# Performance work log

Measured on AMD Instinct MI355X. Metric: run time of the kernel, lower is better.

The kernel has to match this reference:

```python
import jax, jax.numpy as jnp
import numpy as np

B, S, D, H = 2, 2048, 1024, 16
DK = D // H  # 64


def setup_inputs() -> dict:
    key = jax.random.key(0)
    ks = jax.random.split(key, 5)
    query_input = jax.random.normal(ks[0], (B, S, D), dtype=jnp.float32)
    # additive mask: 1.0 where attention is disallowed (causal upper triangle)
    mask = jnp.triu(jnp.ones((S, S), dtype=jnp.float32), k=1)[None, None, :, :]
    scale = 1.0 / np.sqrt(D)
    wq = jax.random.normal(ks[1], (D, D), dtype=jnp.float32) * scale
    wk = jax.random.normal(ks[2], (D, D), dtype=jnp.float32) * scale
    wv = jax.random.normal(ks[3], (D, D), dtype=jnp.float32) * scale
    wo = jax.random.normal(ks[4], (D, D), dtype=jnp.float32) * scale
    return {"query_input": query_input, "mask": mask, "wq": wq, "wk": wk, "wv": wv, "wo": wo}


def _split_heads(x):
    # [B, S, D] -> [B, H, S, DK]
    b, s, _ = x.shape
    return x.reshape(b, s, H, DK).transpose(0, 2, 1, 3)


def reference(query_input, mask, wq, wk, wv, wo):
    # self-attention: key_input = value_input = query_input
    q = _split_heads(query_input @ wq)  # [B, H, S, DK]
    k = _split_heads(query_input @ wk)
    v = _split_heads(query_input @ wv)
    scores = jnp.einsum('bhqd,bhkd->bhqk', q, k) / jnp.sqrt(jnp.float32(DK))
    scores = scores + mask * (-1e9)
    attn = jax.nn.softmax(scores, axis=-1)
    out = jnp.einsum('bhqk,bhkd->bhqd', attn, v)  # [B, H, S, DK]
    out = out.transpose(0, 2, 1, 3).reshape(query_input.shape[0], -1, D)
    return out @ wo
```

## Files before the change

kernel.cpp:

```cpp
#include <hip/hip_runtime.h>

typedef __attribute__((ext_vector_type(8))) short bf16x8;
typedef __attribute__((ext_vector_type(4))) float f32x4;
typedef __attribute__((ext_vector_type(4))) unsigned short u16x4;

#define S_LEN 2048
#define D_DIM 1024
#define NHEAD 16
#define DK 64
#define BH 32
#define MROWS 4096

__device__ __forceinline__ unsigned short f2bf(float f) {
    unsigned int u = __float_as_uint(f);
    u += 0x7fffu + ((u >> 16) & 1u);
    return (unsigned short)(u >> 16);
}

__device__ __forceinline__ unsigned int pk_bf16(float a, float b) {
    unsigned int r;
    asm("v_cvt_pk_bf16_f32 %0, %1, %2" : "=v"(r) : "v"(a), "v"(b));
    return r;
}

__device__ __forceinline__ float fexp2(float x) {
    return __builtin_amdgcn_exp2f(x);
}

__device__ __forceinline__ void gload16(const void* g, void* l) {
    __builtin_amdgcn_global_load_lds(
        (const __attribute__((address_space(1))) void*)g,
        (__attribute__((address_space(3))) void*)l, 16, 0, 0);
}

__global__ __launch_bounds__(256) void cast_x_kernel(const float* __restrict__ X,
                                                     unsigned short* __restrict__ Xb) {
    int idx = blockIdx.x * 256 + threadIdx.x;
    float4 v = ((const float4*)X)[idx];
    u16x4 o;
    o.x = f2bf(v.x); o.y = f2bf(v.y); o.z = f2bf(v.z); o.w = f2bf(v.w);
    ((u16x4*)Xb)[idx] = o;
}

__global__ __launch_bounds__(256) void wtrans_kernel(const float* __restrict__ wq,
                                                     const float* __restrict__ wk,
                                                     const float* __restrict__ wv,
                                                     const float* __restrict__ wo,
                                                     unsigned short* __restrict__ Wt) {
    int z = blockIdx.z;
    const float* W = (z == 0) ? wq : (z == 1) ? wk : (z == 2) ? wv : wo;
    unsigned short* O = Wt + (size_t)z * D_DIM * D_DIM;
    __shared__ float t[32][33];
    int tx = threadIdx.x, ty = threadIdx.y;
    int bx = blockIdx.x * 32;
    int by = blockIdx.y * 32;
#pragma unroll
    for (int i = 0; i < 4; ++i)
        t[ty + i * 8][tx] = W[(size_t)(by + ty + i * 8) * D_DIM + bx + tx];
    __syncthreads();
#pragma unroll
    for (int i = 0; i < 4; ++i)
        O[(size_t)(bx + ty + i * 8) * D_DIM + by + tx] = f2bf(t[tx][ty + i * 8]);
}

__device__ __forceinline__ void gemm_mainloop(const unsigned short* __restrict__ A,
                                              const unsigned short* __restrict__ Bt,
                                              int K, int m0, int n0,
                                              unsigned short* As, unsigned short* Bs,
                                              f32x4 acc[4][4]) {
    const int tid = threadIdx.x;
    const int lane = tid & 63, wid = tid >> 6;
    const int wr = wid >> 1, wc = wid & 1;
    const int fr = lane & 15, fk = (lane >> 4) * 8;
    const int nt = K >> 5;
#pragma unroll
    for (int c = 0; c < 2; ++c) {
        int idx = c * 256 + tid;
        int row = idx >> 2;
        int col = (idx & 3) * 8;
        int base = (c * 256 + wid * 64) * 8;
        gload16(&A[(size_t)(m0 + row) * K + col], &As[base]);
        gload16(&Bt[(size_t)(n0 + row) * K + col], &Bs[base]);
    }
    __syncthreads();
    int buf = 0;
    for (int t = 0; t < nt; ++t) {
        if (t + 1 < nt) {
            int k0 = (t + 1) * 32;
#pragma unroll
            for (int c = 0; c < 2; ++c) {
                int idx = c * 256 + tid;
                int row = idx >> 2;
                int col = (idx & 3) * 8;
                int base = ((buf ^ 1) * 512 + c * 256 + wid * 64) * 8;
                gload16(&A[(size_t)(m0 + row) * K + k0 + col], &As[base]);
                gload16(&Bt[(size_t)(n0 + row) * K + k0 + col], &Bs[base]);
            }
        }
        const unsigned short* Ab = As + buf * 512 * 8;
        const unsigned short* Bb = Bs + buf * 512 * 8;
        bf16x8 af[4], bfr[4];
#pragma unroll
        for (int i = 0; i < 4; ++i)
            af[i] = *(const bf16x8*)&Ab[(wr * 64 + i * 16 + fr) * 32 + fk];
#pragma unroll
        for (int j = 0; j < 4; ++j)
            bfr[j] = *(const bf16x8*)&Bb[(wc * 64 + j * 16 + fr) * 32 + fk];
#pragma unroll
        for (int i = 0; i < 4; ++i)
#pragma unroll
            for (int j = 0; j < 4; ++j)
                acc[i][j] = __builtin_amdgcn_mfma_f32_16x16x32_bf16(af[i], bfr[j], acc[i][j], 0, 0, 0);
        __syncthreads();
        buf ^= 1;
    }
}

#define QSCALE 0.18033688011112042f
__global__ __launch_bounds__(256) void gemm_qkv_kernel(const unsigned short* __restrict__ Xb,
                                                       const unsigned short* __restrict__ Wt,
                                                       unsigned short* __restrict__ QKV,
                                                       unsigned short* __restrict__ Vtp) {
    __shared__ __align__(16) unsigned short SM[16384];
    unsigned short* As = SM;
    unsigned short* Bs = SM + 8192;
    const unsigned short* Bt = Wt + (size_t)blockIdx.z * D_DIM * D_DIM;
    int m0 = blockIdx.y * 128, n0 = blockIdx.x * 128;
    f32x4 acc[4][4] = {};
    gemm_mainloop(Xb, Bt, D_DIM, m0, n0, As, Bs, acc);
    const int tid = threadIdx.x;
    const int lane = tid & 63, wid = tid >> 6;
    const int wr = wid >> 1, wc = wid & 1;
    const int fr = lane & 15, fkg = lane >> 4;
    if (blockIdx.z == 2) {
        const int b = m0 >> 11;
        const int sbase = m0 & 2047;
#pragma unroll
        for (int p = 0; p < 2; ++p) {
#pragma unroll
            for (int jj = 0; jj < 2; ++jj) {
                int j = 2 * p + jj;
                int rrow = wc * 32 + jj * 16 + fr;
#pragma unroll
                for (int i = 0; i < 4; ++i) {
                    int scol = wr * 64 + i * 16 + fkg * 4;
                    u16x4 w;
                    w.x = f2bf(acc[i][j][0]); w.y = f2bf(acc[i][j][1]);
                    w.z = f2bf(acc[i][j][2]); w.w = f2bf(acc[i][j][3]);
                    *(u16x4*)&SM[rrow * 136 + scol] = w;
                }
            }
            __syncthreads();
            int r2 = tid >> 2;
            int c2 = (tid & 3) * 32;
            int wc2 = r2 >> 5, jj2 = (r2 >> 4) & 1, fr2 = r2 & 15;
            int gn = n0 + wc2 * 64 + (2 * p + jj2) * 16 + fr2;
            int bh = b * NHEAD + (gn >> 6), dk = gn & 63;
            size_t go = ((size_t)bh * DK + dk) * S_LEN + sbase + c2;
#pragma unroll
            for (int k = 0; k < 4; ++k)
                *(uint4*)&Vtp[go + 8 * k] = *(const uint4*)&SM[r2 * 136 + c2 + 8 * k];
            __syncthreads();
        }
    } else {
        unsigned short* Out = QKV + (size_t)blockIdx.z * MROWS * D_DIM;
        const float qs = (blockIdx.z == 0) ? QSCALE : 1.0f;
#pragma unroll
        for (int i = 0; i < 4; ++i)
#pragma unroll
            for (int j = 0; j < 4; ++j)
#pragma unroll
                for (int r = 0; r < 4; ++r) {
                    int gm = m0 + wr * 64 + i * 16 + (lane >> 4) * 4 + r;
                    int gn = n0 + wc * 64 + j * 16 + (lane & 15);
                    Out[(size_t)gm * D_DIM + gn] = f2bf(acc[i][j][r] * qs);
                }
    }
}

__global__ __launch_bounds__(512, 4) void attn_kernel(const unsigned short* __restrict__ QKV,
                                                      const unsigned short* __restrict__ Vt,
                                                      unsigned short* __restrict__ AO) {
    const int bh = blockIdx.x;
    const int y = blockIdx.y;
    const int qi = (y < 8) ? (15 - y) : (y - 8);
    const int tid = threadIdx.x, lane = tid & 63, wid = tid >> 6;
    const int fr = lane & 15, fkg = lane >> 4, fk = fkg * 8;
    const unsigned short* Q = QKV;
    const unsigned short* Kd = QKV + (size_t)MROWS * D_DIM;

    __shared__ __align__(16) unsigned short Ks[128][64];
    __shared__ __align__(16) unsigned short Vs[64][128];
    __shared__ __align__(16) unsigned short Ps[8][16][64];

    const int b = bh >> 4, h = bh & 15;
    const int rsw  = fr & 7;
    const int off0 = (fkg ^ rsw) * 8;
    const int off1 = ((4 + fkg) ^ rsw) * 8;

    const int i0 = tid, i1 = 512 + tid;
    const int kr0 = i0 >> 3, kc0 = ((i0 & 7) ^ (kr0 & 7)) * 8;
    const int kr1 = i1 >> 3, kc1 = ((i1 & 7) ^ (kr1 & 7)) * 8;
    const int vr0 = i0 >> 4, vc0 = ((i0 & 15) ^ (vr0 & 15)) * 8;
    const int vr1 = i1 >> 4, vc1 = ((i1 & 15) ^ (vr1 & 15)) * 8;
    const int sb0 = (wid * 64) * 8;
    const int sb1 = (512 + wid * 64) * 8;

    const int q0 = qi * 128;
    const int qr = q0 + wid * 16;

    bf16x8 qf0 = *(const bf16x8*)&Q[((size_t)(b * S_LEN) + qr + fr) * D_DIM + h * DK + fk];
    bf16x8 qf1 = *(const bf16x8*)&Q[((size_t)(b * S_LEN) + qr + fr) * D_DIM + h * DK + 32 + fk];

    f32x4 o[4] = {};
    float m = -1e30f, l = 0.f;
    const int ntiles = qi + 1;

    const unsigned short* kb = Kd + (size_t)(b * S_LEN) * D_DIM + h * DK;
    const unsigned short* vb = Vt + (size_t)bh * DK * S_LEN;

    gload16(kb + (size_t)kr0 * D_DIM + kc0, &Ks[0][0] + sb0);
    gload16(kb + (size_t)kr1 * D_DIM + kc1, &Ks[0][0] + sb1);
    gload16(vb + (size_t)vr0 * S_LEN + vc0, &Vs[0][0] + sb0);
    gload16(vb + (size_t)vr1 * S_LEN + vc1, &Vs[0][0] + sb1);

    for (int t = 0; t < ntiles; ++t) {
        __syncthreads();

        f32x4 s4[8];
        __builtin_amdgcn_s_setprio(1);
#pragma unroll
        for (int nj = 0; nj < 8; ++nj) {
            const unsigned short* krow = &Ks[nj * 16 + fr][0];
            bf16x8 kf0 = *(const bf16x8*)&krow[off0];
            bf16x8 kf1 = *(const bf16x8*)&krow[off1];
            f32x4 z = {};
            z = __builtin_amdgcn_mfma_f32_16x16x32_bf16(kf0, qf0, z, 0, 0, 0);
            z = __builtin_amdgcn_mfma_f32_16x16x32_bf16(kf1, qf1, z, 0, 0, 0);
            s4[nj] = z;
        }
        __builtin_amdgcn_s_setprio(0);

        if (t == ntiles - 1) {
            const int qoff = wid * 16 + fr;
#pragma unroll
            for (int nj = 0; nj < 8; ++nj)
#pragma unroll
                for (int r = 0; r < 4; ++r)
                    s4[nj][r] = (nj * 16 + fkg * 4 + r > qoff) ? -1e30f : s4[nj][r];
        }

        float mg[8];
#pragma unroll
        for (int nj = 0; nj < 8; ++nj)
            mg[nj] = fmaxf(fmaxf(s4[nj][0], s4[nj][1]), fmaxf(s4[nj][2], s4[nj][3]));
        float mt = fmaxf(fmaxf(fmaxf(mg[0], mg[1]), fmaxf(mg[2], mg[3])),
                         fmaxf(fmaxf(mg[4], mg[5]), fmaxf(mg[6], mg[7])));
        mt = fmaxf(mt, __shfl_xor(mt, 16, 64));
        mt = fmaxf(mt, __shfl_xor(mt, 32, 64));
        if (!__all(mt <= m + 8.0f)) {
            float mn = fmaxf(m, mt);
            float corr = fexp2(m - mn);
            m = mn;
            l *= corr;
            o[0] *= corr; o[1] *= corr; o[2] *= corr; o[3] *= corr;
        }
        float ps = 0.f;
        unsigned int pw[8][2];
#pragma unroll
        for (int nj = 0; nj < 8; ++nj) {
            float p0 = fexp2(s4[nj][0] - m);
            float p1 = fexp2(s4[nj][1] - m);
            float p2 = fexp2(s4[nj][2] - m);
            float p3 = fexp2(s4[nj][3] - m);
            ps += (p0 + p1) + (p2 + p3);
            pw[nj][0] = pk_bf16(p0, p1);
            pw[nj][1] = pk_bf16(p2, p3);
        }
        ps += __shfl_xor(ps, 16, 64);
        ps += __shfl_xor(ps, 32, 64);
        l += ps;

#pragma unroll
        for (int hf = 0; hf < 2; ++hf) {
#pragma unroll
            for (int nj = 0; nj < 4; ++nj) {
                int chunk = nj * 2 + (fkg >> 1);
                int el = (fkg & 1) * 4;
                *(uint2*)&Ps[wid][fr][((chunk ^ rsw) << 3) + el] =
                    make_uint2(pw[hf * 4 + nj][0], pw[hf * 4 + nj][1]);
            }
            bf16x8 pf0 = *(const bf16x8*)&Ps[wid][fr][off0];
            bf16x8 pf1 = *(const bf16x8*)&Ps[wid][fr][off1];
            __builtin_amdgcn_s_setprio(1);
#pragma unroll
            for (int j = 0; j < 4; ++j) {
                const unsigned short* vrow = &Vs[j * 16 + fr][0];
                bf16x8 vf0 = *(const bf16x8*)&vrow[((hf * 8 + fkg) ^ fr) * 8];
                bf16x8 vf1 = *(const bf16x8*)&vrow[((hf * 8 + 4 + fkg) ^ fr) * 8];
                o[j] = __builtin_amdgcn_mfma_f32_16x16x32_bf16(vf0, pf0, o[j], 0, 0, 0);
                o[j] = __builtin_amdgcn_mfma_f32_16x16x32_bf16(vf1, pf1, o[j], 0, 0, 0);
            }
            __builtin_amdgcn_s_setprio(0);
        }

        __syncthreads();
        if (t + 1 < ntiles) {
            const int kt = (t + 1) * 128;
            gload16(kb + (size_t)(kt + kr0) * D_DIM + kc0, &Ks[0][0] + sb0);
            gload16(kb + (size_t)(kt + kr1) * D_DIM + kc1, &Ks[0][0] + sb1);
            gload16(vb + (size_t)vr0 * S_LEN + kt + vc0, &Vs[0][0] + sb0);
            gload16(vb + (size_t)vr1 * S_LEN + kt + vc1, &Vs[0][0] + sb1);
        }
    }

    float inv = 1.0f / l;
    size_t rowoff = ((size_t)(b * S_LEN) + qr + fr) * D_DIM + h * DK;
#pragma unroll
    for (int j = 0; j < 4; ++j) {
        u16x4 w;
        w.x = f2bf(o[j][0] * inv); w.y = f2bf(o[j][1] * inv);
        w.z = f2bf(o[j][2] * inv); w.w = f2bf(o[j][3] * inv);
        *(u16x4*)&AO[rowoff + j * 16 + fkg * 4] = w;
    }
}

__global__ __launch_bounds__(256) void gemm_out_kernel(const unsigned short* __restrict__ AO,
                                                       const unsigned short* __restrict__ Wot,
                                                       float* __restrict__ out) {
    __shared__ __align__(16) unsigned short As[2 * 128 * 32];
    __shared__ __align__(16) unsigned short Bs[2 * 128 * 32];
    int m0 = blockIdx.y * 128, n0 = blockIdx.x * 128;
    f32x4 acc[4][4] = {};
    gemm_mainloop(AO, Wot, D_DIM, m0, n0, As, Bs, acc);
    const int lane = threadIdx.x & 63, wid = threadIdx.x >> 6;
    const int wr = wid >> 1, wc = wid & 1;
#pragma unroll
    for (int i = 0; i < 4; ++i)
#pragma unroll
        for (int j = 0; j < 4; ++j)
#pragma unroll
            for (int r = 0; r < 4; ++r) {
                int gm = m0 + wr * 64 + i * 16 + (lane >> 4) * 4 + r;
                int gn = n0 + wc * 64 + j * 16 + (lane & 15);
                out[(size_t)gm * D_DIM + gn] = acc[i][j][r];
            }
}

extern "C" void kernel_launch(void* const* d_in, const int* in_sizes, int n_in,
                              void* d_out, int out_size, void* d_ws, size_t ws_size,
                              hipStream_t stream) {
    (void)in_sizes; (void)n_in; (void)out_size; (void)ws_size;
    const float* X  = (const float*)d_in[0];
    const float* wq = (const float*)d_in[2];
    const float* wk = (const float*)d_in[3];
    const float* wv = (const float*)d_in[4];
    const float* wo = (const float*)d_in[5];

    char* ws = (char*)d_ws;
    unsigned short* Xb  = (unsigned short*)(ws);
    unsigned short* Wt  = (unsigned short*)(ws + ((size_t)8  << 20));
    unsigned short* QKV = (unsigned short*)(ws + ((size_t)16 << 20));
    unsigned short* Vt  = (unsigned short*)(ws + ((size_t)40 << 20));
    unsigned short* AO  = (unsigned short*)(ws + ((size_t)48 << 20));
    float* out = (float*)d_out;

    cast_x_kernel<<<4096, 256, 0, stream>>>(X, Xb);
    wtrans_kernel<<<dim3(32, 32, 4), dim3(32, 8), 0, stream>>>(wq, wk, wv, wo, Wt);
    gemm_qkv_kernel<<<dim3(8, 32, 3), 256, 0, stream>>>(Xb, Wt, QKV, Vt);
    attn_kernel<<<dim3(32, 16), 512, 0, stream>>>(QKV, Vt, AO);
    gemm_out_kernel<<<dim3(8, 32), 256, 0, stream>>>(AO, Wt + (size_t)3 * D_DIM * D_DIM, out);
}
```

Before: 114.8 us.

## Merge prep kernels and single-buffer GEMM LDS to raise occupancy

Folds the X cast and the weight transpose/cast into one prep kernel, saving a launch. It also switches the GEMM main loop from double-buffered async LDS loads to a single buffer guarded by two barriers per k-step, halving shared memory per block so more blocks can be resident. In exchange, global loads no longer overlap with MFMA compute inside a block and each iteration carries an extra barrier. A sync is added before the V epilogue reuses the shared buffer.

```diff
diff --git a/kernel.cpp b/kernel.cpp
--- a/kernel.cpp
+++ b/kernel.cpp
@@ -33,27 +33,31 @@
         (__attribute__((address_space(3))) void*)l, 16, 0, 0);
 }
 
-__global__ __launch_bounds__(256) void cast_x_kernel(const float* __restrict__ X,
-                                                     unsigned short* __restrict__ Xb) {
-    int idx = blockIdx.x * 256 + threadIdx.x;
-    float4 v = ((const float4*)X)[idx];
-    u16x4 o;
-    o.x = f2bf(v.x); o.y = f2bf(v.y); o.z = f2bf(v.z); o.w = f2bf(v.w);
-    ((u16x4*)Xb)[idx] = o;
-}
-
-__global__ __launch_bounds__(256) void wtrans_kernel(const float* __restrict__ wq,
-                                                     const float* __restrict__ wk,
-                                                     const float* __restrict__ wv,
-                                                     const float* __restrict__ wo,
-                                                     unsigned short* __restrict__ Wt) {
-    int z = blockIdx.z;
+__global__ __launch_bounds__(256) void prep_kernel(const float* __restrict__ X,
+                                                   const float* __restrict__ wq,
+                                                   const float* __restrict__ wk,
+                                                   const float* __restrict__ wv,
+                                                   const float* __restrict__ wo,
+                                                   unsigned short* __restrict__ Xb,
+                                                   unsigned short* __restrict__ Wt) {
+    const int bid = blockIdx.x, tid = threadIdx.x;
+    if (bid < 4096) {
+        int idx = bid * 256 + tid;
+        float4 v = ((const float4*)X)[idx];
+        u16x4 o;
+        o.x = f2bf(v.x); o.y = f2bf(v.y); o.z = f2bf(v.z); o.w = f2bf(v.w);
+        ((u16x4*)Xb)[idx] = o;
+        return;
+    }
+    int zb = bid - 4096;
+    int z = zb >> 10;
     const float* W = (z == 0) ? wq : (z == 1) ? wk : (z == 2) ? wv : wo;
     unsigned short* O = Wt + (size_t)z * D_DIM * D_DIM;
     __shared__ float t[32][33];
-    int tx = threadIdx.x, ty = threadIdx.y;
-    int bx = blockIdx.x * 32;
-    int by = blockIdx.y * 32;
+    int t2 = zb & 1023;
+    int bx = (t2 & 31) * 32;
+    int by = (t2 >> 5) * 32;
+    int tx = tid & 31, ty = tid >> 5;
 #pragma unroll
     for (int i = 0; i < 4; ++i)
         t[ty + i * 8][tx] = W[(size_t)(by + ty + i * 8) * D_DIM + bx + tx];
@@ -72,47 +76,30 @@
     const int lane = tid & 63, wid = tid >> 6;
     const int wr = wid >> 1, wc = wid & 1;
     const int fr = lane & 15, fk = (lane >> 4) * 8;
-    const int nt = K >> 5;
-#pragma unroll
-    for (int c = 0; c < 2; ++c) {
-        int idx = c * 256 + tid;
-        int row = idx >> 2;
-        int col = (idx & 3) * 8;
-        int base = (c * 256 + wid * 64) * 8;
-        gload16(&A[(size_t)(m0 + row) * K + col], &As[base]);
-        gload16(&Bt[(size_t)(n0 + row) * K + col], &Bs[base]);
-    }
-    __syncthreads();
-    int buf = 0;
-    for (int t = 0; t < nt; ++t) {
-        if (t + 1 < nt) {
-            int k0 = (t + 1) * 32;
-#pragma unroll
-            for (int c = 0; c < 2; ++c) {
-                int idx = c * 256 + tid;
-                int row = idx >> 2;
-                int col = (idx & 3) * 8;
-                int base = ((buf ^ 1) * 512 + c * 256 + wid * 64) * 8;
-                gload16(&A[(size_t)(m0 + row) * K + k0 + col], &As[base]);
-                gload16(&Bt[(size_t)(n0 + row) * K + k0 + col], &Bs[base]);
-            }
-        }
-        const unsigned short* Ab = As + buf * 512 * 8;
-        const unsigned short* Bb = Bs + buf * 512 * 8;
+    for (int k0 = 0; k0 < K; k0 += 32) {
+        __syncthreads();
+#pragma unroll
+        for (int c = 0; c < 2; ++c) {
+            int idx = c * 256 + tid;
+            int row = idx >> 2;
+            int col = (idx & 3) * 8;
+            int base = (c * 256 + wid * 64) * 8;
+            gload16(&A[(size_t)(m0 + row) * K + k0 + col], &As[base]);
+            gload16(&Bt[(size_t)(n0 + row) * K + k0 + col], &Bs[base]);
+        }
+        __syncthreads();
         bf16x8 af[4], bfr[4];
 #pragma unroll
         for (int i = 0; i < 4; ++i)
-            af[i] = *(const bf16x8*)&Ab[(wr * 64 + i * 16 + fr) * 32 + fk];
+            af[i] = *(const bf16x8*)&As[(wr * 64 + i * 16 + fr) * 32 + fk];
 #pragma unroll
         for (int j = 0; j < 4; ++j)
-            bfr[j] = *(const bf16x8*)&Bb[(wc * 64 + j * 16 + fr) * 32 + fk];
+            bfr[j] = *(const bf16x8*)&Bs[(wc * 64 + j * 16 + fr) * 32 + fk];
 #pragma unroll
         for (int i = 0; i < 4; ++i)
 #pragma unroll
             for (int j = 0; j < 4; ++j)
                 acc[i][j] = __builtin_amdgcn_mfma_f32_16x16x32_bf16(af[i], bfr[j], acc[i][j], 0, 0, 0);
-        __syncthreads();
-        buf ^= 1;
     }
 }
 
@@ -121,9 +108,9 @@
                                                        const unsigned short* __restrict__ Wt,
                                                        unsigned short* __restrict__ QKV,
                                                        unsigned short* __restrict__ Vtp) {
-    __shared__ __align__(16) unsigned short SM[16384];
+    __shared__ __align__(16) unsigned short SM[8704];
     unsigned short* As = SM;
-    unsigned short* Bs = SM + 8192;
+    unsigned short* Bs = SM + 4096;
     const unsigned short* Bt = Wt + (size_t)blockIdx.z * D_DIM * D_DIM;
     int m0 = blockIdx.y * 128, n0 = blockIdx.x * 128;
     f32x4 acc[4][4] = {};
@@ -135,6 +122,7 @@
     if (blockIdx.z == 2) {
         const int b = m0 >> 11;
         const int sbase = m0 & 2047;
+        __syncthreads();
 #pragma unroll
         for (int p = 0; p < 2; ++p) {
 #pragma unroll
@@ -328,8 +316,8 @@
 __global__ __launch_bounds__(256) void gemm_out_kernel(const unsigned short* __restrict__ AO,
                                                        const unsigned short* __restrict__ Wot,
                                                        float* __restrict__ out) {
-    __shared__ __align__(16) unsigned short As[2 * 128 * 32];
-    __shared__ __align__(16) unsigned short Bs[2 * 128 * 32];
+    __shared__ __align__(16) unsigned short As[128 * 32];
+    __shared__ __align__(16) unsigned short Bs[128 * 32];
     int m0 = blockIdx.y * 128, n0 = blockIdx.x * 128;
     f32x4 acc[4][4] = {};
     gemm_mainloop(AO, Wot, D_DIM, m0, n0, As, Bs, acc);
@@ -365,8 +353,7 @@
     unsigned short* AO  = (unsigned short*)(ws + ((size_t)48 << 20));
     float* out = (float*)d_out;
 
-    cast_x_kernel<<<4096, 256, 0, stream>>>(X, Xb);
-    wtrans_kernel<<<dim3(32, 32, 4), dim3(32, 8), 0, stream>>>(wq, wk, wv, wo, Wt);
+    prep_kernel<<<8192, 256, 0, stream>>>(X, wq, wk, wv, wo, Xb, Wt);
     gemm_qkv_kernel<<<dim3(8, 32, 3), 256, 0, stream>>>(Xb, Wt, QKV, Vt);
     attn_kernel<<<dim3(32, 16), 512, 0, stream>>>(QKV, Vt, AO);
     gemm_out_kernel<<<dim3(8, 32), 256, 0, stream>>>(AO, Wt + (size_t)3 * D_DIM * D_DIM, out);
```

Measured after the change: 121.8 us. 6.1% more time.

## Double-buffer K/V tiles in attention and merge prep kernels into one launch

Applied to the files above, without the earlier changes.

The attention kernel now keeps two LDS buffers for K and V. It prefetches the next tile at the top of each iteration so the global loads overlap the current tile's MFMA and softmax work, which leaves one barrier per iteration. The X cast and weight transpose kernels are merged into a single prep launch to save one launch overhead. LDS per block grows from about 48KB to 80KB, which may lower occupancy against the 4-block launch bound.

```diff
diff --git a/kernel.cpp b/kernel.cpp
--- a/kernel.cpp
+++ b/kernel.cpp
@@ -33,27 +33,31 @@
         (__attribute__((address_space(3))) void*)l, 16, 0, 0);
 }
 
-__global__ __launch_bounds__(256) void cast_x_kernel(const float* __restrict__ X,
-                                                     unsigned short* __restrict__ Xb) {
-    int idx = blockIdx.x * 256 + threadIdx.x;
-    float4 v = ((const float4*)X)[idx];
-    u16x4 o;
-    o.x = f2bf(v.x); o.y = f2bf(v.y); o.z = f2bf(v.z); o.w = f2bf(v.w);
-    ((u16x4*)Xb)[idx] = o;
-}
-
-__global__ __launch_bounds__(256) void wtrans_kernel(const float* __restrict__ wq,
-                                                     const float* __restrict__ wk,
-                                                     const float* __restrict__ wv,
-                                                     const float* __restrict__ wo,
-                                                     unsigned short* __restrict__ Wt) {
-    int z = blockIdx.z;
+__global__ __launch_bounds__(256) void prep_kernel(const float* __restrict__ X,
+                                                   const float* __restrict__ wq,
+                                                   const float* __restrict__ wk,
+                                                   const float* __restrict__ wv,
+                                                   const float* __restrict__ wo,
+                                                   unsigned short* __restrict__ Xb,
+                                                   unsigned short* __restrict__ Wt) {
+    const int bid = blockIdx.x, tid = threadIdx.x;
+    if (bid < 4096) {
+        int idx = bid * 256 + tid;
+        float4 v = ((const float4*)X)[idx];
+        u16x4 o;
+        o.x = f2bf(v.x); o.y = f2bf(v.y); o.z = f2bf(v.z); o.w = f2bf(v.w);
+        ((u16x4*)Xb)[idx] = o;
+        return;
+    }
+    int zb = bid - 4096;
+    int z = zb >> 10;
     const float* W = (z == 0) ? wq : (z == 1) ? wk : (z == 2) ? wv : wo;
     unsigned short* O = Wt + (size_t)z * D_DIM * D_DIM;
     __shared__ float t[32][33];
-    int tx = threadIdx.x, ty = threadIdx.y;
-    int bx = blockIdx.x * 32;
-    int by = blockIdx.y * 32;
+    int t2 = zb & 1023;
+    int bx = (t2 & 31) * 32;
+    int by = (t2 >> 5) * 32;
+    int tx = tid & 31, ty = tid >> 5;
 #pragma unroll
     for (int i = 0; i < 4; ++i)
         t[ty + i * 8][tx] = W[(size_t)(by + ty + i * 8) * D_DIM + bx + tx];
@@ -189,8 +193,8 @@
     const unsigned short* Q = QKV;
     const unsigned short* Kd = QKV + (size_t)MROWS * D_DIM;
 
-    __shared__ __align__(16) unsigned short Ks[128][64];
-    __shared__ __align__(16) unsigned short Vs[64][128];
+    __shared__ __align__(16) unsigned short Ks[2][128][64];
+    __shared__ __align__(16) unsigned short Vs[2][64][128];
     __shared__ __align__(16) unsigned short Ps[8][16][64];
 
     const int b = bh >> 4, h = bh & 15;
@@ -219,19 +223,27 @@
     const unsigned short* kb = Kd + (size_t)(b * S_LEN) * D_DIM + h * DK;
     const unsigned short* vb = Vt + (size_t)bh * DK * S_LEN;
 
-    gload16(kb + (size_t)kr0 * D_DIM + kc0, &Ks[0][0] + sb0);
-    gload16(kb + (size_t)kr1 * D_DIM + kc1, &Ks[0][0] + sb1);
-    gload16(vb + (size_t)vr0 * S_LEN + vc0, &Vs[0][0] + sb0);
-    gload16(vb + (size_t)vr1 * S_LEN + vc1, &Vs[0][0] + sb1);
+    gload16(kb + (size_t)kr0 * D_DIM + kc0, &Ks[0][0][0] + sb0);
+    gload16(kb + (size_t)kr1 * D_DIM + kc1, &Ks[0][0][0] + sb1);
+    gload16(vb + (size_t)vr0 * S_LEN + vc0, &Vs[0][0][0] + sb0);
+    gload16(vb + (size_t)vr1 * S_LEN + vc1, &Vs[0][0][0] + sb1);
+    __syncthreads();
 
     for (int t = 0; t < ntiles; ++t) {
-        __syncthreads();
+        const int buf = t & 1;
+        if (t + 1 < ntiles) {
+            const int kt = (t + 1) * 128;
+            gload16(kb + (size_t)(kt + kr0) * D_DIM + kc0, &Ks[buf ^ 1][0][0] + sb0);
+            gload16(kb + (size_t)(kt + kr1) * D_DIM + kc1, &Ks[buf ^ 1][0][0] + sb1);
+            gload16(vb + (size_t)vr0 * S_LEN + kt + vc0, &Vs[buf ^ 1][0][0] + sb0);
+            gload16(vb + (size_t)vr1 * S_LEN + kt + vc1, &Vs[buf ^ 1][0][0] + sb1);
+        }
 
         f32x4 s4[8];
         __builtin_amdgcn_s_setprio(1);
 #pragma unroll
         for (int nj = 0; nj < 8; ++nj) {
-            const unsigned short* krow = &Ks[nj * 16 + fr][0];
+            const unsigned short* krow = &Ks[buf][nj * 16 + fr][0];
             bf16x8 kf0 = *(const bf16x8*)&krow[off0];
             bf16x8 kf1 = *(const bf16x8*)&krow[off1];
             f32x4 z = {};
@@ -295,7 +307,7 @@
             __builtin_amdgcn_s_setprio(1);
 #pragma unroll
             for (int j = 0; j < 4; ++j) {
-                const unsigned short* vrow = &Vs[j * 16 + fr][0];
+                const unsigned short* vrow = &Vs[buf][j * 16 + fr][0];
                 bf16x8 vf0 = *(const bf16x8*)&vrow[((hf * 8 + fkg) ^ fr) * 8];
                 bf16x8 vf1 = *(const bf16x8*)&vrow[((hf * 8 + 4 + fkg) ^ fr) * 8];
                 o[j] = __builtin_amdgcn_mfma_f32_16x16x32_bf16(vf0, pf0, o[j], 0, 0, 0);
@@ -305,13 +317,6 @@
         }
 
         __syncthreads();
-        if (t + 1 < ntiles) {
-            const int kt = (t + 1) * 128;
-            gload16(kb + (size_t)(kt + kr0) * D_DIM + kc0, &Ks[0][0] + sb0);
-            gload16(kb + (size_t)(kt + kr1) * D_DIM + kc1, &Ks[0][0] + sb1);
-            gload16(vb + (size_t)vr0 * S_LEN + kt + vc0, &Vs[0][0] + sb0);
-            gload16(vb + (size_t)vr1 * S_LEN + kt + vc1, &Vs[0][0] + sb1);
-        }
     }
 
     float inv = 1.0f / l;
@@ -365,8 +370,7 @@
     unsigned short* AO  = (unsigned short*)(ws + ((size_t)48 << 20));
     float* out = (float*)d_out;
 
-    cast_x_kernel<<<4096, 256, 0, stream>>>(X, Xb);
-    wtrans_kernel<<<dim3(32, 32, 4), dim3(32, 8), 0, stream>>>(wq, wk, wv, wo, Wt);
+    prep_kernel<<<8192, 256, 0, stream>>>(X, wq, wk, wv, wo, Xb, Wt);
     gemm_qkv_kernel<<<dim3(8, 32, 3), 256, 0, stream>>>(Xb, Wt, QKV, Vt);
     attn_kernel<<<dim3(32, 16), 512, 0, stream>>>(QKV, Vt, AO);
     gemm_out_kernel<<<dim3(8, 32), 256, 0, stream>>>(AO, Wt + (size_t)3 * D_DIM * D_DIM, out);
```

New measurement: 114.3 us. No clear change (-0.5%).
